# Kernel optimization log

Measured on AMD Instinct MI355X. Metric: run time of the kernel, lower is better.

## Reference

```python
import jax, jax.numpy as jnp
import numpy as np

# thresholds from options['dist_threshold'] (init-time constants)
THRESHOLDS = jnp.array([0.5, 1.0], dtype=jnp.float32)

B, N, D, K = 16, 16384, 64, 64  # batch, h*w pixels, embed dim, n templates
N_CLASSES = 21


def setup_inputs() -> dict:
    key = jax.random.key(0)
    k1, k2, k3 = jax.random.split(key, 3)
    frame_embeddings = jax.random.normal(k1, (B, N, D), dtype=jnp.float32)
    templates = jax.random.normal(k2, (K, N, D), dtype=jnp.float32)
    template_classes = jax.random.randint(k3, (K,), 0, N_CLASSES, dtype=jnp.int64)
    return {
        "frame_embeddings": frame_embeddings,
        "templates": templates,
        "template_classes": template_classes,
    }


def reference(frame_embeddings, templates, template_classes):
    # Squared euclidean distance per pixel to each template, vectorized over K
    # [B,K,N,D] broadcast intermediate the torch loop also never materializes).
    x2 = jnp.sum(frame_embeddings * frame_embeddings, axis=-1)      # [B, N]
    t2 = jnp.sum(templates * templates, axis=-1)                    # [K, N]
    xt = jnp.einsum('bnd,knd->bkn', frame_embeddings, templates)    # [B, K, N]
    dists = x2[:, None, :] + t2[None, :, :] - 2.0 * xt              # [B, K, N]

    min_dists = jnp.min(dists, axis=1)                              # [B, N]
    min_idx = jnp.argmin(dists, axis=1)                             # [B, N]

    # One boolean mask per threshold, stacked: [T, B, N]
    masks = min_dists[None, :, :] <= THRESHOLDS[:, None, None]
    pred_classes = template_classes[min_idx]                        # [B, N]
    return masks, min_dists, pred_classes
```

## Files before the change

kernel.cpp:

```cpp
#include <hip/hip_runtime.h>
#include <stdint.h>


#define BB 16
#define NN 16384
#define DD 64
#define KK 64

typedef float v2f __attribute__((ext_vector_type(2)));

__global__ __launch_bounds__(512, 6)
void openset_kernel(const float* __restrict__ x,
                    const float* __restrict__ tmpl,
                    const int*   __restrict__ tcls,
                    float*       __restrict__ out) {
    __shared__ float4 st[KK * 32];
    __shared__ float4 sx[BB * 32];

    const int lane = threadIdx.x & 63;
    const int wv   = threadIdx.x >> 6;
    const int pp   = wv & 1;
    const int q    = wv >> 1;
    const int p0   = (int)(((blockIdx.x & 7) << 11) | ((blockIdx.x >> 3) << 1));

    const int half = lane >> 5;
    const int i32  = lane & 31;

#pragma unroll
    for (int c = 0; c < 4; ++c) {
        const int k = (wv * 4 + c) * 2 + half;
        const float4* src =
            (const float4*)(tmpl + ((size_t)k << 20)) + (size_t)p0 * 16;
        st[k * 32 + (i32 ^ (k & 7))] = src[i32];
    }
    {
        const int b = wv * 2 + half;
        const float4* src =
            (const float4*)(x + ((size_t)b << 20)) + (size_t)p0 * 16;
        sx[b * 32 + i32] = src[i32];
    }
    __syncthreads();

    v2f acc[4];
#pragma unroll
    for (int i = 0; i < 4; ++i) acc[i] = (v2f){0.f, 0.f};

#pragma unroll
    for (int h = 0; h < 2; ++h) {
        v2f a0[4], a1[4];
#pragma unroll
        for (int i = 0; i < 4; ++i) { a0[i] = (v2f){0.f, 0.f}; a1[i] = (v2f){0.f, 0.f}; }
#pragma unroll
        for (int j = 0; j < 8; ++j) {
            const int e = pp * 16 + h * 8 + j;
            const float4 tv = st[lane * 32 + (e ^ (lane & 7))];
#pragma unroll
            for (int i = 0; i < 4; ++i) {
                const float4 xv = sx[(q * 4 + i) * 32 + e];
                v2f d0 = (v2f){xv.x - tv.x, xv.y - tv.y};
                v2f d1 = (v2f){xv.z - tv.z, xv.w - tv.w};
                a0[i] += d0 * d0;
                a1[i] += d1 * d1;
            }
        }
#pragma unroll
        for (int i = 0; i < 4; ++i) acc[i] += a0[i] + a1[i];
    }

    float bestd = 0.f;
    int   bestk = 0;
#pragma unroll
    for (int i = 0; i < 4; ++i) {
        const float dme = acc[i].x + acc[i].y;
        float m = dme;
#pragma unroll
        for (int s = 1; s < 64; s <<= 1)
            m = fminf(m, __shfl_xor(m, s));
        const unsigned long long tie = __ballot(dme == m);
        const int ks = __ffsll(tie) - 1;
        if (lane == i) { bestd = m; bestk = ks; }
    }

    if (lane < 4) {
        const int b = q * 4 + lane;
        const size_t BN = (size_t)BB * NN;
        const size_t o  = (size_t)b * NN + (p0 + pp);
        out[o]          = (bestd <= 0.5f) ? 1.0f : 0.0f;
        out[BN + o]     = (bestd <= 1.0f) ? 1.0f : 0.0f;
        out[2 * BN + o] = bestd;
        out[3 * BN + o] = (float)tcls[bestk];
    }
}

extern "C" void kernel_launch(void* const* d_in, const int* in_sizes, int n_in,
                              void* d_out, int out_size, void* d_ws, size_t ws_size,
                              hipStream_t stream) {
    const float* x    = (const float*)d_in[0];
    const float* tmpl = (const float*)d_in[1];
    const int*   tcls = (const int*)d_in[2];
    float* out = (float*)d_out;

    dim3 grid(NN / 2);
    dim3 block(512);
    openset_kernel<<<grid, block, 0, stream>>>(x, tmpl, tcls, out);
}
```

Baseline: 400.4 us.

## Double-buffer tile loads via global_load_lds across four pixel-pair tiles per block

Each block now handles four consecutive pixel-pair tiles instead of one. It loads templates and embeddings directly into LDS with global_load_lds, so the data skips registers, and it double-buffers so the next tile's loads overlap the current tile's compute. The grid shrinks fourfold and the occupancy hint drops from 6 to 4 blocks per CU because LDS per block doubles. There is a risk of a race: the only __syncthreads sits at the end of each tile, and the code issues no explicit wait (vmcnt) on the async LDS loads before reading the next buffer.

```diff
diff --git a/kernel.cpp b/kernel.cpp
--- a/kernel.cpp
+++ b/kernel.cpp
@@ -6,89 +6,114 @@
 #define NN 16384
 #define DD 64
 #define KK 64
+#define TILES 4
 
 typedef float v2f __attribute__((ext_vector_type(2)));
 
-__global__ __launch_bounds__(512, 6)
+__device__ __forceinline__ void gll16(const void* g, void* l) {
+    __builtin_amdgcn_global_load_lds(
+        (const __attribute__((address_space(1))) void*)g,
+        (__attribute__((address_space(3))) void*)l, 16, 0, 0);
+}
+
+__global__ __launch_bounds__(512, 4)
 void openset_kernel(const float* __restrict__ x,
                     const float* __restrict__ tmpl,
                     const int*   __restrict__ tcls,
                     float*       __restrict__ out) {
-    __shared__ float4 st[KK * 32];
-    __shared__ float4 sx[BB * 32];
+    __shared__ float4 st[2][KK * 32];
+    __shared__ float4 sx[2][BB * 32];
 
     const int lane = threadIdx.x & 63;
     const int wv   = threadIdx.x >> 6;
     const int pp   = wv & 1;
     const int q    = wv >> 1;
-    const int p0   = (int)(((blockIdx.x & 7) << 11) | ((blockIdx.x >> 3) << 1));
-
     const int half = lane >> 5;
     const int i32  = lane & 31;
 
+    const int p0b = (int)(((blockIdx.x & 7) << 11) | ((blockIdx.x >> 3) << 3));
+
+    const float4* tsrc[4];
 #pragma unroll
     for (int c = 0; c < 4; ++c) {
         const int k = (wv * 4 + c) * 2 + half;
-        const float4* src =
-            (const float4*)(tmpl + ((size_t)k << 20)) + (size_t)p0 * 16;
-        st[k * 32 + (i32 ^ (k & 7))] = src[i32];
+        tsrc[c] = (const float4*)(tmpl + ((size_t)k << 20))
+                  + (size_t)p0b * 16 + (i32 ^ (k & 7));
     }
-    {
-        const int b = wv * 2 + half;
-        const float4* src =
-            (const float4*)(x + ((size_t)b << 20)) + (size_t)p0 * 16;
-        sx[b * 32 + i32] = src[i32];
-    }
+    const float4* xsrc = (const float4*)(x + ((size_t)(wv * 2 + half) << 20))
+                         + (size_t)p0b * 16 + i32;
+
+#pragma unroll
+    for (int c = 0; c < 4; ++c) gll16(tsrc[c], &st[0][(wv * 4 + c) * 64]);
+    gll16(xsrc, &sx[0][wv * 64]);
     __syncthreads();
 
-    v2f acc[4];
 #pragma unroll
-    for (int i = 0; i < 4; ++i) acc[i] = (v2f){0.f, 0.f};
+    for (int t = 0; t < TILES; ++t) {
+        const int cur = t & 1;
+
+        if (t + 1 < TILES) {
+            const int nxt = cur ^ 1;
+#pragma unroll
+            for (int c = 0; c < 4; ++c)
+                gll16(tsrc[c] + (t + 1) * 32, &st[nxt][(wv * 4 + c) * 64]);
+            gll16(xsrc + (t + 1) * 32, &sx[nxt][wv * 64]);
+        }
+
+        v2f acc[4];
+#pragma unroll
+        for (int i = 0; i < 4; ++i) acc[i] = (v2f){0.f, 0.f};
 
 #pragma unroll
-    for (int h = 0; h < 2; ++h) {
-        v2f a0[4], a1[4];
-#pragma unroll
-        for (int i = 0; i < 4; ++i) { a0[i] = (v2f){0.f, 0.f}; a1[i] = (v2f){0.f, 0.f}; }
-#pragma unroll
-        for (int j = 0; j < 8; ++j) {
-            const int e = pp * 16 + h * 8 + j;
-            const float4 tv = st[lane * 32 + (e ^ (lane & 7))];
+        for (int h = 0; h < 2; ++h) {
+            v2f a0[4], a1[4];
 #pragma unroll
             for (int i = 0; i < 4; ++i) {
-                const float4 xv = sx[(q * 4 + i) * 32 + e];
-                v2f d0 = (v2f){xv.x - tv.x, xv.y - tv.y};
-                v2f d1 = (v2f){xv.z - tv.z, xv.w - tv.w};
-                a0[i] += d0 * d0;
-                a1[i] += d1 * d1;
+                a0[i] = (v2f){0.f, 0.f};
+                a1[i] = (v2f){0.f, 0.f};
             }
+#pragma unroll
+            for (int j = 0; j < 8; ++j) {
+                const int e = pp * 16 + h * 8 + j;
+                const float4 tv = st[cur][lane * 32 + (e ^ (lane & 7))];
+#pragma unroll
+                for (int i = 0; i < 4; ++i) {
+                    const float4 xv = sx[cur][(q * 4 + i) * 32 + e];
+                    v2f d0 = (v2f){xv.x - tv.x, xv.y - tv.y};
+                    v2f d1 = (v2f){xv.z - tv.z, xv.w - tv.w};
+                    a0[i] += d0 * d0;
+                    a1[i] += d1 * d1;
+                }
+            }
+#pragma unroll
+            for (int i = 0; i < 4; ++i) acc[i] += a0[i] + a1[i];
         }
+
+        float bestd = 0.f;
+        int   bestk = 0;
 #pragma unroll
-        for (int i = 0; i < 4; ++i) acc[i] += a0[i] + a1[i];
-    }
+        for (int i = 0; i < 4; ++i) {
+            const float dme = acc[i].x + acc[i].y;
+            float m = dme;
+#pragma unroll
+            for (int s = 1; s < 64; s <<= 1)
+                m = fminf(m, __shfl_xor(m, s));
+            const unsigned long long tie = __ballot(dme == m);
+            const int ks = __ffsll(tie) - 1;
+            if (lane == i) { bestd = m; bestk = ks; }
+        }
 
-    float bestd = 0.f;
-    int   bestk = 0;
-#pragma unroll
-    for (int i = 0; i < 4; ++i) {
-        const float dme = acc[i].x + acc[i].y;
-        float m = dme;
-#pragma unroll
-        for (int s = 1; s < 64; s <<= 1)
-            m = fminf(m, __shfl_xor(m, s));
-        const unsigned long long tie = __ballot(dme == m);
-        const int ks = __ffsll(tie) - 1;
-        if (lane == i) { bestd = m; bestk = ks; }
-    }
+        if (lane < 4) {
+            const int b = q * 4 + lane;
+            const size_t BN = (size_t)BB * NN;
+            const size_t o  = (size_t)b * NN + (p0b + 2 * t + pp);
+            out[o]          = (bestd <= 0.5f) ? 1.0f : 0.0f;
+            out[BN + o]     = (bestd <= 1.0f) ? 1.0f : 0.0f;
+            out[2 * BN + o] = bestd;
+            out[3 * BN + o] = (float)tcls[bestk];
+        }
 
-    if (lane < 4) {
-        const int b = q * 4 + lane;
-        const size_t BN = (size_t)BB * NN;
-        const size_t o  = (size_t)b * NN + (p0 + pp);
-        out[o]          = (bestd <= 0.5f) ? 1.0f : 0.0f;
-        out[BN + o]     = (bestd <= 1.0f) ? 1.0f : 0.0f;
-        out[2 * BN + o] = bestd;
-        out[3 * BN + o] = (float)tcls[bestk];
+        __syncthreads();
     }
 }
 
@@ -100,7 +125,7 @@
     const int*   tcls = (const int*)d_in[2];
     float* out = (float*)d_out;
 
-    dim3 grid(NN / 2);
+    dim3 grid(NN / (2 * TILES));
     dim3 block(512);
     openset_kernel<<<grid, block, 0, stream>>>(x, tmpl, tcls, out);
 }
```

After: 409.7 us. 2.3% more time.
